# Performance work log

Measured on AMD Instinct MI355X. Metric: run time of the kernel, lower is better.

The kernel has to match this reference:

```python
import jax, jax.numpy as jnp
import numpy as np

N = 500000      # total nodes
C = 256         # channels
R = 4           # reduction
B = 1024        # number of graphs (segments)


def setup_inputs() -> dict:
    key = jax.random.key(0)
    k1, k2, k3, k4 = jax.random.split(key, 4)
    x = jax.random.normal(k1, (N, C), dtype=jnp.float32)
    batch = jnp.sort(jax.random.randint(k2, (N,), 0, B, dtype=jnp.int64))
    # shared MLP weights (Linear without bias); stored as [in, out] for x @ W
    w1 = jax.random.normal(k3, (C, C // R), dtype=jnp.float32) * (1.0 / np.sqrt(C))
    w2 = jax.random.normal(k4, (C // R, C), dtype=jnp.float32) * (1.0 / np.sqrt(C // R))
    return {"x": x, "batch": batch, "w1": w1, "w2": w2}


def reference(x, batch, w1, w2):
    # scatter reductions over graph ids (dim_size = B)
    sum_res = jax.ops.segment_sum(x, batch, num_segments=B)          # [B, C]
    max_res = jax.ops.segment_max(x, batch, num_segments=B)          # [B, C]
    counts = jax.ops.segment_sum(jnp.ones((x.shape[0],), x.dtype), batch, num_segments=B)
    # torch_scatter fills empty segments with 0; segment_max gives -inf
    max_res = jnp.where(counts[:, None] > 0, max_res, jnp.zeros_like(max_res))

    def mlp(h):  # shared bottleneck MLP: Linear -> ReLU -> Linear (no bias)
        return jnp.maximum(h @ w1, 0) @ w2

    y = jax.nn.relu(mlp(max_res) + mlp(sum_res))                     # [B, C]
    return x * y[batch]                                              # gather + gate
```

## Files before the change

kernel.cpp:

```cpp
#include <hip/hip_runtime.h>
#include <math.h>

#define CCH   256
#define CCH4  64
#define BSEG  1024
#define HID   64

__global__ __launch_bounds__(256) void seg_reduce_kernel(
    const float* __restrict__ x, const int* __restrict__ batch, int N,
    float* __restrict__ sum_res, float* __restrict__ max_res) {
  int seg = blockIdx.x;
  __shared__ int s_bounds[2];
  if (threadIdx.x < 2) {
    int tgt = seg + (int)threadIdx.x;
    int lo = 0, hi = N;
    while (lo < hi) {
      int mid = (lo + hi) >> 1;
      if (batch[mid] < tgt) lo = mid + 1; else hi = mid;
    }
    s_bounds[threadIdx.x] = lo;
  }
  __syncthreads();
  int start = s_bounds[0], end = s_bounds[1];

  int wave = threadIdx.x >> 6;
  int lane = threadIdx.x & 63;
  const float4* x4 = (const float4*)x;

  float4 s = make_float4(0.f, 0.f, 0.f, 0.f);
  float4 m = make_float4(-INFINITY, -INFINITY, -INFINITY, -INFINITY);
  for (int r = start + wave; r < end; r += 4) {
    float4 v = x4[(size_t)r * CCH4 + lane];
    s.x += v.x; s.y += v.y; s.z += v.z; s.w += v.w;
    m.x = fmaxf(m.x, v.x); m.y = fmaxf(m.y, v.y);
    m.z = fmaxf(m.z, v.z); m.w = fmaxf(m.w, v.w);
  }

  __shared__ float4 sh_s[4][CCH4];
  __shared__ float4 sh_m[4][CCH4];
  sh_s[wave][lane] = s;
  sh_m[wave][lane] = m;
  __syncthreads();

  if (wave == 0) {
    float4 ts = sh_s[0][lane];
    float4 tm = sh_m[0][lane];
    for (int w = 1; w < 4; ++w) {
      float4 os = sh_s[w][lane];
      float4 om = sh_m[w][lane];
      ts.x += os.x; ts.y += os.y; ts.z += os.z; ts.w += os.w;
      tm.x = fmaxf(tm.x, om.x); tm.y = fmaxf(tm.y, om.y);
      tm.z = fmaxf(tm.z, om.z); tm.w = fmaxf(tm.w, om.w);
    }
    if (start == end) tm = make_float4(0.f, 0.f, 0.f, 0.f);
    ((float4*)sum_res)[(size_t)seg * CCH4 + lane] = ts;
    ((float4*)max_res)[(size_t)seg * CCH4 + lane] = tm;
  }
}

__global__ __launch_bounds__(256) void mlp_kernel(
    const float* __restrict__ sum_res, const float* __restrict__ max_res,
    const float* __restrict__ w1, const float* __restrict__ w2,
    float* __restrict__ y) {
  int seg = blockIdx.x;
  int t = threadIdx.x;
  __shared__ float srow[CCH];
  __shared__ float mrow[CCH];
  __shared__ float hsum[HID];
  __shared__ float hmax[HID];

  srow[t] = sum_res[(size_t)seg * CCH + t];
  mrow[t] = max_res[(size_t)seg * CCH + t];
  __syncthreads();

  if (t < HID) {
    float acc = 0.f;
    #pragma unroll 8
    for (int k = 0; k < CCH; ++k) acc = fmaf(srow[k], w1[k * HID + t], acc);
    hsum[t] = fmaxf(acc, 0.f);
  } else if (t < 2 * HID) {
    int j = t - HID;
    float acc = 0.f;
    #pragma unroll 8
    for (int k = 0; k < CCH; ++k) acc = fmaf(mrow[k], w1[k * HID + j], acc);
    hmax[j] = fmaxf(acc, 0.f);
  }
  __syncthreads();

  float acc = 0.f;
  #pragma unroll 8
  for (int j = 0; j < HID; ++j) acc = fmaf(hsum[j] + hmax[j], w2[j * CCH + t], acc);
  y[(size_t)seg * CCH + t] = fmaxf(acc, 0.f);
}

__global__ __launch_bounds__(256) void gate_kernel(
    const float* __restrict__ x, const int* __restrict__ batch,
    const float* __restrict__ y, float* __restrict__ out, int total4) {
  int idx = blockIdx.x * blockDim.x + threadIdx.x;
  if (idx >= total4) return;
  int n = idx >> 6;
  int q = idx & 63;
  int b = batch[n];
  const float4* x4 = (const float4*)x;
  const float4* y4 = (const float4*)y;
  float4 xv = x4[idx];
  float4 yv = y4[b * CCH4 + q];
  float4 o;
  o.x = xv.x * yv.x; o.y = xv.y * yv.y; o.z = xv.z * yv.z; o.w = xv.w * yv.w;
  ((float4*)out)[idx] = o;
}

extern "C" void kernel_launch(void* const* d_in, const int* in_sizes, int n_in,
                              void* d_out, int out_size, void* d_ws, size_t ws_size,
                              hipStream_t stream) {
  const float* x     = (const float*)d_in[0];
  const int*   batch = (const int*)d_in[1];
  const float* w1    = (const float*)d_in[2];
  const float* w2    = (const float*)d_in[3];
  float* out = (float*)d_out;

  int N = in_sizes[1];

  float* sum_res = (float*)d_ws;
  float* max_res = sum_res + (size_t)BSEG * CCH;
  float* y       = max_res + (size_t)BSEG * CCH;

  seg_reduce_kernel<<<BSEG, 256, 0, stream>>>(x, batch, N, sum_res, max_res);
  mlp_kernel<<<BSEG, 256, 0, stream>>>(sum_res, max_res, w1, w2, y);

  int total4 = N * CCH4;
  int blocks = (total4 + 255) / 256;
  gate_kernel<<<blocks, 256, 0, stream>>>(x, batch, y, out, total4);
}
```

Measured before the change: 930.4 us.

## Parallelize segment reduction over fixed row chunks with atomic sum/max

Replaces the one-block-per-segment reduction, which gave only 1024 blocks with about 490 rows each, with a grid of waves that each handle 64 contiguous rows. Partial results are combined into a zeroed workspace with float atomicAdd for sums and an order-preserving unsigned encoding with atomicMax for maxima. The MLP kernel decodes the max keys and maps key 0 (empty segment) to 0. This adds a memset, many global atomics, and nondeterministic float summation order.

```diff
diff --git a/kernel.cpp b/kernel.cpp
--- a/kernel.cpp
+++ b/kernel.cpp
@@ -5,61 +5,75 @@
 #define CCH4  64
 #define BSEG  1024
 #define HID   64
+#define RPW   64
+
+__device__ __forceinline__ unsigned enc_f32(float f) {
+  unsigned u = __float_as_uint(f);
+  return (u & 0x80000000u) ? ~u : (u | 0x80000000u);
+}
+__device__ __forceinline__ float dec_f32(unsigned u) {
+  return (u & 0x80000000u) ? __uint_as_float(u & 0x7fffffffu)
+                           : __uint_as_float(~u);
+}
 
 __global__ __launch_bounds__(256) void seg_reduce_kernel(
     const float* __restrict__ x, const int* __restrict__ batch, int N,
-    float* __restrict__ sum_res, float* __restrict__ max_res) {
-  int seg = blockIdx.x;
-  __shared__ int s_bounds[2];
-  if (threadIdx.x < 2) {
-    int tgt = seg + (int)threadIdx.x;
-    int lo = 0, hi = N;
-    while (lo < hi) {
-      int mid = (lo + hi) >> 1;
-      if (batch[mid] < tgt) lo = mid + 1; else hi = mid;
-    }
-    s_bounds[threadIdx.x] = lo;
-  }
-  __syncthreads();
-  int start = s_bounds[0], end = s_bounds[1];
+    float* __restrict__ sum_res, unsigned* __restrict__ max_keys) {
+  int wave = (blockIdx.x << 2) | (threadIdx.x >> 6);
+  int lane = threadIdx.x & 63;
+  int start = wave * RPW;
+  if (start >= N) return;
+  int cnt = min(RPW, N - start);
 
-  int wave = threadIdx.x >> 6;
-  int lane = threadIdx.x & 63;
+  int bv = batch[min(start + lane, N - 1)];
+  int b_first = __shfl(bv, 0);
+  int b_last  = __shfl(bv, cnt - 1);
+
   const float4* x4 = (const float4*)x;
+  const float4* xp = x4 + (size_t)start * CCH4 + lane;
 
   float4 s = make_float4(0.f, 0.f, 0.f, 0.f);
   float4 m = make_float4(-INFINITY, -INFINITY, -INFINITY, -INFINITY);
-  for (int r = start + wave; r < end; r += 4) {
-    float4 v = x4[(size_t)r * CCH4 + lane];
-    s.x += v.x; s.y += v.y; s.z += v.z; s.w += v.w;
-    m.x = fmaxf(m.x, v.x); m.y = fmaxf(m.y, v.y);
-    m.z = fmaxf(m.z, v.z); m.w = fmaxf(m.w, v.w);
-  }
 
-  __shared__ float4 sh_s[4][CCH4];
-  __shared__ float4 sh_m[4][CCH4];
-  sh_s[wave][lane] = s;
-  sh_m[wave][lane] = m;
-  __syncthreads();
+  auto flush = [&](int seg) {
+    float* sp = sum_res + (size_t)seg * CCH + (lane << 2);
+    unsigned* mp = max_keys + (size_t)seg * CCH + (lane << 2);
+    atomicAdd(sp + 0, s.x); atomicAdd(sp + 1, s.y);
+    atomicAdd(sp + 2, s.z); atomicAdd(sp + 3, s.w);
+    atomicMax(mp + 0, enc_f32(m.x)); atomicMax(mp + 1, enc_f32(m.y));
+    atomicMax(mp + 2, enc_f32(m.z)); atomicMax(mp + 3, enc_f32(m.w));
+  };
 
-  if (wave == 0) {
-    float4 ts = sh_s[0][lane];
-    float4 tm = sh_m[0][lane];
-    for (int w = 1; w < 4; ++w) {
-      float4 os = sh_s[w][lane];
-      float4 om = sh_m[w][lane];
-      ts.x += os.x; ts.y += os.y; ts.z += os.z; ts.w += os.w;
-      tm.x = fmaxf(tm.x, om.x); tm.y = fmaxf(tm.y, om.y);
-      tm.z = fmaxf(tm.z, om.z); tm.w = fmaxf(tm.w, om.w);
+  if (b_first == b_last && cnt == RPW) {
+    #pragma unroll 8
+    for (int r = 0; r < RPW; ++r) {
+      float4 v = xp[(size_t)r * CCH4];
+      s.x += v.x; s.y += v.y; s.z += v.z; s.w += v.w;
+      m.x = fmaxf(m.x, v.x); m.y = fmaxf(m.y, v.y);
+      m.z = fmaxf(m.z, v.z); m.w = fmaxf(m.w, v.w);
     }
-    if (start == end) tm = make_float4(0.f, 0.f, 0.f, 0.f);
-    ((float4*)sum_res)[(size_t)seg * CCH4 + lane] = ts;
-    ((float4*)max_res)[(size_t)seg * CCH4 + lane] = tm;
+    flush(b_first);
+  } else {
+    int cur = b_first;
+    for (int r = 0; r < cnt; ++r) {
+      int b = __shfl(bv, r);
+      if (b != cur) {
+        flush(cur);
+        cur = b;
+        s = make_float4(0.f, 0.f, 0.f, 0.f);
+        m = make_float4(-INFINITY, -INFINITY, -INFINITY, -INFINITY);
+      }
+      float4 v = xp[(size_t)r * CCH4];
+      s.x += v.x; s.y += v.y; s.z += v.z; s.w += v.w;
+      m.x = fmaxf(m.x, v.x); m.y = fmaxf(m.y, v.y);
+      m.z = fmaxf(m.z, v.z); m.w = fmaxf(m.w, v.w);
+    }
+    flush(cur);
   }
 }
 
 __global__ __launch_bounds__(256) void mlp_kernel(
-    const float* __restrict__ sum_res, const float* __restrict__ max_res,
+    const float* __restrict__ sum_res, const unsigned* __restrict__ max_keys,
     const float* __restrict__ w1, const float* __restrict__ w2,
     float* __restrict__ y) {
   int seg = blockIdx.x;
@@ -70,7 +84,8 @@
   __shared__ float hmax[HID];
 
   srow[t] = sum_res[(size_t)seg * CCH + t];
-  mrow[t] = max_res[(size_t)seg * CCH + t];
+  unsigned key = max_keys[(size_t)seg * CCH + t];
+  mrow[t] = (key == 0u) ? 0.f : dec_f32(key);
   __syncthreads();
 
   if (t < HID) {
@@ -121,14 +136,18 @@
 
   int N = in_sizes[1];
 
-  float* sum_res = (float*)d_ws;
-  float* max_res = sum_res + (size_t)BSEG * CCH;
-  float* y       = max_res + (size_t)BSEG * CCH;
+  float*    sum_res  = (float*)d_ws;
+  unsigned* max_keys = (unsigned*)(sum_res + (size_t)BSEG * CCH);
+  float*    y        = (float*)(max_keys + (size_t)BSEG * CCH);
 
-  seg_reduce_kernel<<<BSEG, 256, 0, stream>>>(x, batch, N, sum_res, max_res);
-  mlp_kernel<<<BSEG, 256, 0, stream>>>(sum_res, max_res, w1, w2, y);
+  hipMemsetAsync(d_ws, 0, (size_t)2 * BSEG * CCH * sizeof(float), stream);
+
+  int waves  = (N + RPW - 1) / RPW;
+  int blocks = (waves + 3) / 4;
+  seg_reduce_kernel<<<blocks, 256, 0, stream>>>(x, batch, N, sum_res, max_keys);
+  mlp_kernel<<<BSEG, 256, 0, stream>>>(sum_res, max_keys, w1, w2, y);
 
   int total4 = N * CCH4;
-  int blocks = (total4 + 255) / 256;
-  gate_kernel<<<blocks, 256, 0, stream>>>(x, batch, y, out, total4);
+  int gblocks = (total4 + 255) / 256;
+  gate_kernel<<<gblocks, 256, 0, stream>>>(x, batch, y, out, total4);
 }
```

New measurement: 946.6 us. About the same (+1.7%).
